# Kernel tuning notes

Measured on AMD Instinct MI355X. Metric: run time of the kernel, lower is better.

## Reference

```python
import jax, jax.numpy as jnp
import numpy as np

B, N, D, K, H, L = 4, 20000, 64, 256, 4, 2
F = 4 * D
DH = D // H
SCALE = DH ** -0.5
EPS = 1e-5


def _layernorm(x, g, b):
    m = jnp.mean(x, axis=-1, keepdims=True)
    v = jnp.mean(jnp.square(x - m), axis=-1, keepdims=True)
    return (x - m) / jnp.sqrt(v + EPS) * g + b


def setup_inputs() -> dict:
    key = jax.random.key(0)
    ks = jax.random.split(key, 12)
    s = 0.02
    return {
        'expr': jax.random.normal(ks[0], (B, N), jnp.float32),
        'emb': jax.random.normal(ks[1], (N, D), jnp.float32),
        'Wq': jax.random.normal(ks[2], (L, D, D), jnp.float32) * s,
        'Wk': jax.random.normal(ks[3], (L, D, D), jnp.float32) * s,
        'Wv': jax.random.normal(ks[4], (L, D, D), jnp.float32) * s,
        'projK': jax.random.normal(ks[5], (L, N, K), jnp.float32) * s,
        'projV': jax.random.normal(ks[6], (L, N, K), jnp.float32) * s,
        'Wo': jax.random.normal(ks[7], (L, D, D), jnp.float32) * s,
        'bo': jnp.zeros((L, D), jnp.float32),
        'g1': jnp.ones((L, D), jnp.float32),
        'be1': jnp.zeros((L, D), jnp.float32),
        'W1': jax.random.normal(ks[8], (L, D, F), jnp.float32) * s,
        'bf1': jnp.zeros((L, F), jnp.float32),
        'W2': jax.random.normal(ks[9], (L, F, D), jnp.float32) * s,
        'bf2': jnp.zeros((L, D), jnp.float32),
        'g2': jnp.ones((L, D), jnp.float32),
        'be2': jnp.zeros((L, D), jnp.float32),
    }


def _forward(expr, emb, Wq, Wk, Wv, projK, projV, Wo, bo, g1, be1, W1, bf1, W2, bf2, g2, be2):
    # gene_ids = arange(N) for every batch row -> embedding lookup is just the table
    x = emb[None, :, :] * expr[:, :, None]  # [B, N, D]
    for i in range(L):
        b = x.shape[0]
        # Linformer self-attention
        q = jnp.einsum('bnd,de->bne', x, Wq[i])                 # [B, N, D]
        k_low = jnp.einsum('bnd,nk->bkd', x, projK[i])          # [B, K, D]
        v_low = jnp.einsum('bnd,nk->bkd', x, projV[i])          # [B, K, D]
        k = jnp.einsum('bkd,de->bke', k_low, Wk[i])             # [B, K, D]
        v = jnp.einsum('bkd,de->bke', v_low, Wv[i])             # [B, K, D]
        qh = q.reshape(b, N, H, DH).transpose(0, 2, 1, 3)       # [B, H, N, DH]
        kh = k.reshape(b, K, H, DH).transpose(0, 2, 1, 3)       # [B, H, K, DH]
        vh = v.reshape(b, K, H, DH).transpose(0, 2, 1, 3)       # [B, H, K, DH]
        dots = jnp.einsum('bhnd,bhkd->bhnk', qh, kh) * SCALE    # [B, H, N, K]
        attn = jax.nn.softmax(dots, axis=-1)
        o = jnp.einsum('bhnk,bhkd->bhnd', attn, vh)             # [B, H, N, DH]
        o = o.transpose(0, 2, 1, 3).reshape(b, N, D)
        o = jnp.einsum('bnd,de->bne', o, Wo[i]) + bo[i]
        x = _layernorm(o + x, g1[i], be1[i])
        # FFN (exact GELU, matching torch nn.GELU default)
        h = jax.nn.gelu(jnp.einsum('bnd,df->bnf', x, W1[i]) + bf1[i], approximate=False)
        f = jnp.einsum('bnf,fd->bnd', h, W2[i]) + bf2[i]
        x = _layernorm(f + x, g2[i], be2[i])
    return x


def reference(expr, emb, Wq, Wk, Wv, projK, projV, Wo, bo, g1, be1, W1, bf1, W2, bf2, g2, be2):
    return _forward(expr, emb, Wq, Wk, Wv, projK, projV, Wo, bo, g1, be1, W1, bf1, W2, bf2, g2, be2)
```

## Files before the change

kernel.cpp:

```cpp
#include <hip/hip_runtime.h>

using u16 = unsigned short;
typedef __bf16 bf16x8 __attribute__((ext_vector_type(8)));
typedef u16    u16x8  __attribute__((ext_vector_type(8)));
typedef u16    u16x4  __attribute__((ext_vector_type(4)));
typedef float  f32x4  __attribute__((ext_vector_type(4)));
typedef float  f32x16 __attribute__((ext_vector_type(16)));

#define DEV static __device__ __forceinline__

constexpr int NB = 4;
constexpr int NN = 20000;
constexpr int DD = 64;
constexpr int KK = 256;
constexpr int ROWS = NB * NN;

DEV float b2f(u16 u) { union { unsigned i; float f; } c; c.i = ((unsigned)u) << 16; return c.f; }
DEV u16 f2b(float f) {
  union { float f; unsigned i; } c; c.f = f;
  unsigned i = c.i + 0x7FFFu + ((c.i >> 16) & 1u);
  return (u16)(i >> 16);
}
DEV bf16x8 ldb8(const u16* p) { return *reinterpret_cast<const bf16x8*>(p); }
DEV f32x16 mfma32(bf16x8 a, bf16x8 b, f32x16 c) { return __builtin_amdgcn_mfma_f32_32x32x16_bf16(a, b, c, 0, 0, 0); }

__global__ __launch_bounds__(256) void k_wconv(
    const float* __restrict__ Wq, const float* __restrict__ Wo,
    const float* __restrict__ W1, const float* __restrict__ W2, u16* __restrict__ wb) {
  int m = blockIdx.y, l = blockIdx.z;
  const float* src; u16* dst; int Dout, S, CT;
  if (m == 0)      { src = Wq + l * 4096;  dst = wb + l * 4096;          Dout = 64;  S = 4;  CT = 2; }
  else if (m == 1) { src = Wo + l * 4096;  dst = wb + 8192 + l * 4096;   Dout = 64;  S = 4;  CT = 2; }
  else if (m == 2) { src = W1 + l * 16384; dst = wb + 16384 + l * 16384; Dout = 256; S = 4;  CT = 8; }
  else             { src = W2 + l * 16384; dst = wb + 49152 + l * 16384; Dout = 64;  S = 16; CT = 2; }
  int slot = blockIdx.x * 256 + threadIdx.x;
  if (slot >= S * CT * 64) return;
  int s = slot / (CT * 64), rem = slot % (CT * 64);
  int ct = rem >> 6, lane = rem & 63;
  int hi = lane >> 5, lo = lane & 31;
  u16x8 o;
#pragma unroll
  for (int j = 0; j < 8; ++j) o[j] = f2b(src[(s * 16 + hi * 8 + j) * Dout + ct * 32 + lo]);
  *reinterpret_cast<u16x8*>(&dst[slot * 8]) = o;
}

__global__ __launch_bounds__(256) void k_transpose(
    const float* __restrict__ projK, const float* __restrict__ projV,
    u16* __restrict__ pKT, u16* __restrict__ pVT) {
  int nt = blockIdx.x, kt = blockIdx.y, z = blockIdx.z;
  int layer = z & 1, pv = z >> 1;
  const float* src = (pv ? projV : projK) + (size_t)layer * NN * KK;
  u16* dst = (pv ? pVT : pKT) + (size_t)layer * KK * NN;
  int n0 = nt * 64, k0 = kt * 64;
  __shared__ float lds[64][65];
  int t = threadIdx.x;
  int r = t >> 4, c4 = (t & 15) * 4;
#pragma unroll
  for (int i = 0; i < 4; ++i) {
    int rr = r + i * 16;
    float4 v = make_float4(0.f, 0.f, 0.f, 0.f);
    if (n0 + rr < NN) v = *reinterpret_cast<const float4*>(&src[(size_t)(n0 + rr) * KK + k0 + c4]);
    lds[c4 + 0][rr] = v.x; lds[c4 + 1][rr] = v.y; lds[c4 + 2][rr] = v.z; lds[c4 + 3][rr] = v.w;
  }
  __syncthreads();
  int kr = t >> 3, nb = (t & 7) * 8;
#pragma unroll
  for (int p = 0; p < 2; ++p) {
    int k = kr + p * 32;
    if (n0 + nb < NN) {
      u16x8 o;
#pragma unroll
      for (int j = 0; j < 8; ++j) o[j] = f2b(lds[k][nb + j]);
      *reinterpret_cast<u16x8*>(&dst[(size_t)(k0 + k) * NN + n0 + nb]) = o;
    }
  }
}

__global__ __launch_bounds__(256) void k_xt(const u16* __restrict__ x, u16* __restrict__ xT) {
  int nt = blockIdx.x, b = blockIdx.y;
  int n0 = nt * 64;
  __shared__ u16 lds[64][70];
  int t = threadIdx.x;
  int r = t >> 4, c4 = (t & 15) * 4;
  const u16* xb = x + (size_t)b * NN * 64;
#pragma unroll
  for (int i = 0; i < 4; ++i) {
    int rr = r + i * 16;
    u16x4 v = {};
    if (n0 + rr < NN) v = *reinterpret_cast<const u16x4*>(&xb[(size_t)(n0 + rr) * 64 + c4]);
    lds[c4 + 0][rr] = v[0]; lds[c4 + 1][rr] = v[1];
    lds[c4 + 2][rr] = v[2]; lds[c4 + 3][rr] = v[3];
  }
  __syncthreads();
  int dr = t >> 3, nb = (t & 7) * 8;
  u16* xo = xT + (size_t)b * 64 * NN;
#pragma unroll
  for (int p = 0; p < 2; ++p) {
    int d = dr + p * 32;
    if (n0 + nb < NN) {
      u16x8 o;
#pragma unroll
      for (int j = 0; j < 8; ++j) o[j] = lds[d][nb + j];
      *reinterpret_cast<u16x8*>(&xo[(size_t)d * NN + n0 + nb]) = o;
    }
  }
}

__global__ __launch_bounds__(256) void k_embed(
    const float* __restrict__ expr, const float* __restrict__ emb, u16* __restrict__ xb) {
  int idx8 = (blockIdx.x * 256 + threadIdx.x) * 8;
  int b = idx8 / (NN * DD);
  int rem = idx8 - b * (NN * DD);
  int n = rem >> 6, d = rem & 63;
  float4 e0 = *reinterpret_cast<const float4*>(&emb[(n << 6) + d]);
  float4 e1 = *reinterpret_cast<const float4*>(&emb[(n << 6) + d + 4]);
  float s = expr[b * NN + n];
  u16x8 o;
  o[0] = f2b(e0.x * s); o[1] = f2b(e0.y * s); o[2] = f2b(e0.z * s); o[3] = f2b(e0.w * s);
  o[4] = f2b(e1.x * s); o[5] = f2b(e1.y * s); o[6] = f2b(e1.z * s); o[7] = f2b(e1.w * s);
  *reinterpret_cast<u16x8*>(&xb[idx8]) = o;
}

template <int EPI>
__global__ __launch_bounds__(256) void k_gemm_64_64(
    const u16* __restrict__ A, const u16* __restrict__ WB,
    const float* __restrict__ bias, const u16* __restrict__ res,
    const float* __restrict__ g, const float* __restrict__ be, u16* __restrict__ out) {
  int t = threadIdx.x, w = t >> 6, lane = t & 63;
  int lo = lane & 31, hi = lane >> 5;
  int unit = blockIdx.x * 4 + w;
  if (unit >= ROWS / 64) return;
  bf16x8 wf[4][2];
#pragma unroll
  for (int s = 0; s < 4; ++s)
#pragma unroll
    for (int ct = 0; ct < 2; ++ct) wf[s][ct] = ldb8(&WB[((s * 2 + ct) * 64 + lane) * 8]);
  float bia[2], gg[2], bb[2];
  if (EPI) {
#pragma unroll
    for (int ct = 0; ct < 2; ++ct) {
      bia[ct] = bias[ct * 32 + lo];
      gg[ct] = g[ct * 32 + lo];
      bb[ct] = be[ct * 32 + lo];
    }
  }
  f32x16 acc[2][2] = {};
  int r0 = unit * 64;
#pragma unroll
  for (int s = 0; s < 4; ++s) {
#pragma unroll
    for (int rt = 0; rt < 2; ++rt) {
      bf16x8 a = ldb8(&A[(size_t)(r0 + rt * 32 + lo) * 64 + s * 16 + hi * 8]);
      acc[rt][0] = mfma32(a, wf[s][0], acc[rt][0]);
      acc[rt][1] = mfma32(a, wf[s][1], acc[rt][1]);
    }
  }
#pragma unroll
  for (int rt = 0; rt < 2; ++rt) {
#pragma unroll
    for (int reg = 0; reg < 16; ++reg) {
      int row = r0 + rt * 32 + (reg & 3) + 8 * (reg >> 2) + 4 * hi;
      if (EPI == 0) {
        out[(size_t)row * 64 + lo] = f2b(acc[rt][0][reg]);
        out[(size_t)row * 64 + 32 + lo] = f2b(acc[rt][1][reg]);
      } else {
        float a0 = acc[rt][0][reg] + bia[0] + b2f(res[(size_t)row * 64 + lo]);
        float a1 = acc[rt][1][reg] + bia[1] + b2f(res[(size_t)row * 64 + 32 + lo]);
        float su = a0 + a1, sq = a0 * a0 + a1 * a1;
#pragma unroll
        for (int m = 1; m <= 16; m <<= 1) { su += __shfl_xor(su, m); sq += __shfl_xor(sq, m); }
        float mean = su * (1.f / 64.f);
        float var = sq * (1.f / 64.f) - mean * mean;
        float rstd = rsqrtf(var + 1e-5f);
        out[(size_t)row * 64 + lo] = f2b((a0 - mean) * rstd * gg[0] + bb[0]);
        out[(size_t)row * 64 + 32 + lo] = f2b((a1 - mean) * rstd * gg[1] + bb[1]);
      }
    }
  }
}

__global__ __launch_bounds__(256, 2) void k_gemm_64_256(
    const u16* __restrict__ A, const u16* __restrict__ WB,
    const float* __restrict__ bias, u16* __restrict__ out) {
  int t = threadIdx.x, w = t >> 6, lane = t & 63;
  int lo = lane & 31, hi = lane >> 5;
  int colg = w & 1;
  int unit = blockIdx.x * 2 + (w >> 1);
  if (unit >= ROWS / 32) return;
  bf16x8 wf[4][4];
  float bia[4];
#pragma unroll
  for (int s = 0; s < 4; ++s)
#pragma unroll
    for (int ct = 0; ct < 4; ++ct) wf[s][ct] = ldb8(&WB[((s * 8 + colg * 4 + ct) * 64 + lane) * 8]);
#pragma unroll
  for (int ct = 0; ct < 4; ++ct) bia[ct] = bias[colg * 128 + ct * 32 + lo];
  f32x16 acc[4] = {};
  int r0 = unit * 32;
#pragma unroll
  for (int s = 0; s < 4; ++s) {
    bf16x8 a = ldb8(&A[(size_t)(r0 + lo) * 64 + s * 16 + hi * 8]);
#pragma unroll
    for (int ct = 0; ct < 4; ++ct) acc[ct] = mfma32(a, wf[s][ct], acc[ct]);
  }
#pragma unroll
  for (int ct = 0; ct < 4; ++ct) {
#pragma unroll
    for (int reg = 0; reg < 16; ++reg) {
      int row = r0 + (reg & 3) + 8 * (reg >> 2) + 4 * hi;
      float x = acc[ct][reg] + bia[ct];
      float gel = 0.5f * x * (1.f + erff(x * 0.7071067811865475f));
      out[(size_t)row * 256 + colg * 128 + ct * 32 + lo] = f2b(gel);
    }
  }
}

__global__ __launch_bounds__(256) void k_gemm_256_64(
    const u16* __restrict__ A, const u16* __restrict__ WB,
    const float* __restrict__ bias, const u16* __restrict__ res,
    const float* __restrict__ g, const float* __restrict__ be,
    u16* __restrict__ outb, float* __restrict__ outf) {
  int t = threadIdx.x, w = t >> 6, lane = t & 63;
  int lo = lane & 31, hi = lane >> 5;
  int unit = blockIdx.x * 4 + w;
  if (unit >= ROWS / 64) return;
  float bia[2], gg[2], bb[2];
#pragma unroll
  for (int ct = 0; ct < 2; ++ct) {
    bia[ct] = bias[ct * 32 + lo];
    gg[ct] = g[ct * 32 + lo];
    bb[ct] = be[ct * 32 + lo];
  }
  f32x16 acc[2][2] = {};
  int r0 = unit * 64;
#pragma unroll
  for (int s = 0; s < 16; ++s) {
    bf16x8 w0 = ldb8(&WB[((s * 2 + 0) * 64 + lane) * 8]);
    bf16x8 w1 = ldb8(&WB[((s * 2 + 1) * 64 + lane) * 8]);
#pragma unroll
    for (int rt = 0; rt < 2; ++rt) {
      bf16x8 a = ldb8(&A[(size_t)(r0 + rt * 32 + lo) * 256 + s * 16 + hi * 8]);
      acc[rt][0] = mfma32(a, w0, acc[rt][0]);
      acc[rt][1] = mfma32(a, w1, acc[rt][1]);
    }
  }
#pragma unroll
  for (int rt = 0; rt < 2; ++rt) {
#pragma unroll
    for (int reg = 0; reg < 16; ++reg) {
      int row = r0 + rt * 32 + (reg & 3) + 8 * (reg >> 2) + 4 * hi;
      float a0 = acc[rt][0][reg] + bia[0] + b2f(res[(size_t)row * 64 + lo]);
      float a1 = acc[rt][1][reg] + bia[1] + b2f(res[(size_t)row * 64 + 32 + lo]);
      float su = a0 + a1, sq = a0 * a0 + a1 * a1;
#pragma unroll
      for (int m = 1; m <= 16; m <<= 1) { su += __shfl_xor(su, m); sq += __shfl_xor(sq, m); }
      float mean = su * (1.f / 64.f);
      float var = sq * (1.f / 64.f) - mean * mean;
      float rstd = rsqrtf(var + 1e-5f);
      float o0 = (a0 - mean) * rstd * gg[0] + bb[0];
      float o1 = (a1 - mean) * rstd * gg[1] + bb[1];
      if (outb) {
        outb[(size_t)row * 64 + lo] = f2b(o0);
        outb[(size_t)row * 64 + 32 + lo] = f2b(o1);
      }
      if (outf) {
        outf[(size_t)row * 64 + lo] = o0;
        outf[(size_t)row * 64 + 32 + lo] = o1;
      }
    }
  }
}

__global__ __launch_bounds__(256) void k_proj(
    const u16* __restrict__ xT, const u16* __restrict__ pKT_l, const u16* __restrict__ pVT_l,
    float* __restrict__ part) {
  int c = blockIdx.x, b = blockIdx.y, proj = blockIdx.z;
  const u16* P = proj ? pVT_l : pKT_l;
  int t = threadIdx.x, w = t >> 6, lane = t & 63;
  int lo = lane & 31, hi = lane >> 5;
  int d0 = (w & 1) * 32;
  int kbase = (w >> 1) * 128;
  int n0 = c * 512;
  int rem = NN - n0;
  int steps = (rem < 512 ? rem : 512) >> 4;
  const u16* xr = xT + ((size_t)b * 64 + d0 + lo) * NN;
  f32x16 acc[4] = {};
  for (int s = 0; s < steps; ++s) {
    int nb = n0 + s * 16 + hi * 8;
    bf16x8 a = ldb8(&xr[nb]);
#pragma unroll
    for (int gI = 0; gI < 4; ++gI) {
      bf16x8 bfr = ldb8(&P[(size_t)(kbase + gI * 32 + lo) * NN + nb]);
      acc[gI] = mfma32(a, bfr, acc[gI]);
    }
  }
  float* dst = part + ((size_t)(proj * NB + b) * 40 + c) * (64 * 256);
#pragma unroll
  for (int gI = 0; gI < 4; ++gI)
#pragma unroll
    for (int r = 0; r < 16; ++r) {
      int d = d0 + (r & 3) + 8 * (r >> 2) + 4 * hi;
      dst[d * 256 + kbase + gI * 32 + lo] = acc[gI][r];
    }
}

__global__ __launch_bounds__(256) void k_p2(
    const float* __restrict__ part, const float* __restrict__ Wk_l, const float* __restrict__ Wv_l,
    u16* __restrict__ kbuf, u16* __restrict__ vT) {
  int ks = blockIdx.x, b = blockIdx.y, proj = blockIdx.z;
  int k0 = ks * 8;
  const float* W = proj ? Wv_l : Wk_l;
  __shared__ float low[64][8];
  int t = threadIdx.x;
  const float* src = part + (size_t)(proj * NB + b) * 40 * (64 * 256);
#pragma unroll
  for (int i = 0; i < 2; ++i) {
    int idx = i * 256 + t;
    int e = idx >> 3, k = idx & 7;
    float s = 0.f;
    for (int cc = 0; cc < 40; ++cc) s += src[(size_t)cc * (64 * 256) + e * 256 + k0 + k];
    low[e][k] = s;
  }
  __syncthreads();
#pragma unroll
  for (int i = 0; i < 2; ++i) {
    int idx = i * 256 + t;
    int d = idx & 63, kk = idx >> 6;
    float a = 0.f;
#pragma unroll
    for (int e = 0; e < 64; ++e) a += low[e][kk] * W[e * 64 + d];
    u16 o = f2b(a);
    if (proj == 0)
      kbuf[((size_t)b * KK + k0 + kk) * 64 + d] = o;
    else
      vT[((size_t)b * 64 + d) * KK + k0 + kk] = o;
  }
}

__global__ __launch_bounds__(256) void k_attn(
    const u16* __restrict__ q, const u16* __restrict__ kbuf, const u16* __restrict__ vT,
    u16* __restrict__ ao) {
  int t = threadIdx.x, w = t >> 6, lane = t & 63;
  int lo = lane & 31, hi = lane >> 5;
  int h = blockIdx.y, b = blockIdx.z;
  int n0w = blockIdx.x * 128 + w * 32;
  if (n0w >= NN) return;
  const u16* qb = q + (size_t)b * NN * 64;
  const u16* kb = kbuf + (size_t)b * KK * 64 + h * 16;
  const u16* vtb = vT + (size_t)b * 64 * KK + (size_t)(h * 16 + (lane & 15)) * KK;
  u16* aob = ao + (size_t)b * NN * 64;
  const float C = 0.25f * 1.4426950408889634f;
  bf16x8 qf = ldb8(&qb[(size_t)(n0w + lo) * 64 + h * 16 + hi * 8]);
  f32x16 acc = {};
  float ssum = 0.f;
#pragma unroll
  for (int kt = 0; kt < 8; ++kt) {
    bf16x8 kf = ldb8(&kb[(size_t)(kt * 32 + lo) * 64 + hi * 8]);
    f32x16 z = {};
    f32x16 s = mfma32(kf, qf, z);
#pragma unroll
    for (int r = 0; r < 16; ++r) { s[r] = exp2f(s[r] * C); ssum += s[r]; }
#pragma unroll
    for (int c = 0; c < 2; ++c) {
      float px[8];
#pragma unroll
      for (int j = 0; j < 8; ++j) px[j] = __shfl_xor(s[c * 8 + j], 32);
      u16x8 bu;
#pragma unroll
      for (int j = 0; j < 4; ++j) {
        bu[j] = f2b(hi ? px[4 + j] : s[c * 8 + j]);
        bu[4 + j] = f2b(hi ? s[c * 8 + 4 + j] : px[j]);
      }
      bf16x8 af = ldb8(&vtb[kt * 32 + c * 16 + hi * 8]);
      acc = mfma32(af, __builtin_bit_cast(bf16x8, bu), acc);
    }
  }
  ssum += __shfl_xor(ssum, 32);
  float inv = 1.f / ssum;
  float o[8], ox[8];
#pragma unroll
  for (int r = 0; r < 8; ++r) o[r] = acc[r] * inv;
#pragma unroll
  for (int r = 0; r < 8; ++r) ox[r] = __shfl_xor(o[r], 32);
  u16x8 st;
#pragma unroll
  for (int j = 0; j < 4; ++j) {
    st[j] = f2b(hi ? ox[4 + j] : o[j]);
    st[4 + j] = f2b(hi ? o[4 + j] : ox[j]);
  }
  *reinterpret_cast<u16x8*>(&aob[(size_t)(n0w + lo) * 64 + h * 16 + hi * 8]) = st;
}

extern "C" void kernel_launch(void* const* d_in, const int* in_sizes, int n_in,
                              void* d_out, int out_size, void* d_ws, size_t ws_size,
                              hipStream_t stream) {
  const float* expr = (const float*)d_in[0];
  const float* emb  = (const float*)d_in[1];
  const float* Wq   = (const float*)d_in[2];
  const float* Wk   = (const float*)d_in[3];
  const float* Wv   = (const float*)d_in[4];
  const float* projK = (const float*)d_in[5];
  const float* projV = (const float*)d_in[6];
  const float* Wo   = (const float*)d_in[7];
  const float* bo   = (const float*)d_in[8];
  const float* g1   = (const float*)d_in[9];
  const float* be1  = (const float*)d_in[10];
  const float* W1   = (const float*)d_in[11];
  const float* bf1  = (const float*)d_in[12];
  const float* W2   = (const float*)d_in[13];
  const float* bf2  = (const float*)d_in[14];
  const float* g2   = (const float*)d_in[15];
  const float* be2  = (const float*)d_in[16];
  float* out = (float*)d_out;
  char* ws = (char*)d_ws;

  u16* xb0 = (u16*)(ws + 0);
  u16* xb1 = (u16*)(ws + 10240000);
  u16* xb2 = (u16*)(ws + 20480000);
  u16* qb  = (u16*)(ws + 30720000);
  u16* aob = (u16*)(ws + 40960000);
  u16* hb  = (u16*)(ws + 51200000);
  float* part = (float*)(ws + 51200000);
  u16* pKT = (u16*)(ws + 92160000);
  u16* pVT = (u16*)(ws + 112640000);
  u16* xTb = (u16*)(ws + 133120000);
  u16* kB  = (u16*)(ws + 143360000);
  u16* vTB = (u16*)(ws + 143491072);
  u16* wb  = (u16*)(ws + 143622144);

  k_wconv<<<dim3(8, 4, 2), 256, 0, stream>>>(Wq, Wo, W1, W2, wb);
  k_transpose<<<dim3(313, 4, 4), 256, 0, stream>>>(projK, projV, pKT, pVT);
  k_embed<<<2500, 256, 0, stream>>>(expr, emb, xb0);

  const u16* xin = xb0;
  for (int l = 0; l < 2; ++l) {
    const u16* wbq = wb + l * 4096;
    const u16* wbo = wb + 8192 + l * 4096;
    const u16* wb1 = wb + 16384 + l * 16384;
    const u16* wb2 = wb + 49152 + l * 16384;
    k_gemm_64_64<0><<<313, 256, 0, stream>>>(xin, wbq, nullptr, nullptr, nullptr, nullptr, qb);
    k_xt<<<dim3(313, NB), 256, 0, stream>>>(xin, xTb);
    k_proj<<<dim3(40, NB, 2), 256, 0, stream>>>(xTb, pKT + (size_t)l * KK * NN, pVT + (size_t)l * KK * NN, part);
    k_p2<<<dim3(32, NB, 2), 256, 0, stream>>>(part, Wk + l * 4096, Wv + l * 4096, kB, vTB);
    k_attn<<<dim3(157, 4, NB), 256, 0, stream>>>(qb, kB, vTB, aob);
    k_gemm_64_64<1><<<313, 256, 0, stream>>>(aob, wbo, bo + l * 64, xin, g1 + l * 64, be1 + l * 64, xb1);
    k_gemm_64_256<<<1250, 256, 0, stream>>>(xb1, wb1, bf1 + l * 256, hb);
    k_gemm_256_64<<<313, 256, 0, stream>>>(hb, wb2, bf2 + l * 64, xb1,
                                           g2 + l * 64, be2 + l * 64,
                                           l == 0 ? xb2 : nullptr, l == 1 ? out : nullptr);
    xin = xb2;
  }
}
```

Baseline: 490.3 us.

## Merge preprocessing and Q/transpose kernels, streamline attention softmax, halve GEMM row tiles

Folds the weight conversion, projection transposes and embedding into one k_pre launch, and the Q projection plus x transpose into one k_qxt launch, to cut launch overhead. The attention softmax now uses exp2 with log2e·scale folded into K, packed bf16 conversion and permlane32 swaps. The row sum comes from an extra ones column in the PV MFMA. The k_proj loop is unrolled by 4 to issue more loads up front, and the 64-wide GEMMs move to 32-row units per wave with double the grid. The changes carry some risk: the ones-buffer trick depends on the V layout, and exp2 is used without max subtraction.

```diff
diff --git a/kernel.cpp b/kernel.cpp
--- a/kernel.cpp
+++ b/kernel.cpp
@@ -6,6 +6,7 @@
 typedef u16    u16x4  __attribute__((ext_vector_type(4)));
 typedef float  f32x4  __attribute__((ext_vector_type(4)));
 typedef float  f32x16 __attribute__((ext_vector_type(16)));
+typedef unsigned uint4v __attribute__((ext_vector_type(4)));
 
 #define DEV static __device__ __forceinline__
 
@@ -24,248 +25,140 @@
 DEV bf16x8 ldb8(const u16* p) { return *reinterpret_cast<const bf16x8*>(p); }
 DEV f32x16 mfma32(bf16x8 a, bf16x8 b, f32x16 c) { return __builtin_amdgcn_mfma_f32_32x32x16_bf16(a, b, c, 0, 0, 0); }
 
-__global__ __launch_bounds__(256) void k_wconv(
+DEV unsigned cvtpk(float lo, float hi) {
+  unsigned r;
+  asm("v_cvt_pk_bf16_f32 %0, %1, %2" : "=v"(r) : "v"(lo), "v"(hi));
+  return r;
+}
+DEV void swap32(unsigned& a, unsigned& b) {
+  auto r = __builtin_amdgcn_permlane32_swap((int)a, (int)b, false, false);
+  a = (unsigned)r[0]; b = (unsigned)r[1];
+}
+
+__global__ __launch_bounds__(256) void k_pre(
+    const float* __restrict__ expr, const float* __restrict__ emb,
     const float* __restrict__ Wq, const float* __restrict__ Wo,
-    const float* __restrict__ W1, const float* __restrict__ W2, u16* __restrict__ wb) {
-  int m = blockIdx.y, l = blockIdx.z;
-  const float* src; u16* dst; int Dout, S, CT;
-  if (m == 0)      { src = Wq + l * 4096;  dst = wb + l * 4096;          Dout = 64;  S = 4;  CT = 2; }
-  else if (m == 1) { src = Wo + l * 4096;  dst = wb + 8192 + l * 4096;   Dout = 64;  S = 4;  CT = 2; }
-  else if (m == 2) { src = W1 + l * 16384; dst = wb + 16384 + l * 16384; Dout = 256; S = 4;  CT = 8; }
-  else             { src = W2 + l * 16384; dst = wb + 49152 + l * 16384; Dout = 64;  S = 16; CT = 2; }
-  int slot = blockIdx.x * 256 + threadIdx.x;
-  if (slot >= S * CT * 64) return;
-  int s = slot / (CT * 64), rem = slot % (CT * 64);
-  int ct = rem >> 6, lane = rem & 63;
-  int hi = lane >> 5, lo = lane & 31;
-  u16x8 o;
-#pragma unroll
-  for (int j = 0; j < 8; ++j) o[j] = f2b(src[(s * 16 + hi * 8 + j) * Dout + ct * 32 + lo]);
-  *reinterpret_cast<u16x8*>(&dst[slot * 8]) = o;
-}
-
-__global__ __launch_bounds__(256) void k_transpose(
+    const float* __restrict__ W1, const float* __restrict__ W2,
     const float* __restrict__ projK, const float* __restrict__ projV,
-    u16* __restrict__ pKT, u16* __restrict__ pVT) {
-  int nt = blockIdx.x, kt = blockIdx.y, z = blockIdx.z;
-  int layer = z & 1, pv = z >> 1;
-  const float* src = (pv ? projV : projK) + (size_t)layer * NN * KK;
-  u16* dst = (pv ? pVT : pKT) + (size_t)layer * KK * NN;
-  int n0 = nt * 64, k0 = kt * 64;
+    u16* __restrict__ wb, u16* __restrict__ pKT, u16* __restrict__ pVT,
+    u16* __restrict__ xb, u16* __restrict__ ones) {
   __shared__ float lds[64][65];
+  int bid = blockIdx.x;
   int t = threadIdx.x;
-  int r = t >> 4, c4 = (t & 15) * 4;
-#pragma unroll
-  for (int i = 0; i < 4; ++i) {
-    int rr = r + i * 16;
-    float4 v = make_float4(0.f, 0.f, 0.f, 0.f);
-    if (n0 + rr < NN) v = *reinterpret_cast<const float4*>(&src[(size_t)(n0 + rr) * KK + k0 + c4]);
-    lds[c4 + 0][rr] = v.x; lds[c4 + 1][rr] = v.y; lds[c4 + 2][rr] = v.z; lds[c4 + 3][rr] = v.w;
-  }
-  __syncthreads();
-  int kr = t >> 3, nb = (t & 7) * 8;
-#pragma unroll
-  for (int p = 0; p < 2; ++p) {
-    int k = kr + p * 32;
-    if (n0 + nb < NN) {
-      u16x8 o;
-#pragma unroll
-      for (int j = 0; j < 8; ++j) o[j] = f2b(lds[k][nb + j]);
-      *reinterpret_cast<u16x8*>(&dst[(size_t)(k0 + k) * NN + n0 + nb]) = o;
-    }
-  }
-}
-
-__global__ __launch_bounds__(256) void k_xt(const u16* __restrict__ x, u16* __restrict__ xT) {
-  int nt = blockIdx.x, b = blockIdx.y;
-  int n0 = nt * 64;
-  __shared__ u16 lds[64][70];
+  if (bid < 5008) {
+    int nt = bid % 313, q = bid / 313, kt = q & 3, z = q >> 2;
+    int layer = z & 1, pv = z >> 1;
+    const float* src = (pv ? projV : projK) + (size_t)layer * NN * KK;
+    u16* dst = (pv ? pVT : pKT) + (size_t)layer * KK * NN;
+    int n0 = nt * 64, k0 = kt * 64;
+    int r = t >> 4, c4 = (t & 15) * 4;
+#pragma unroll
+    for (int i = 0; i < 4; ++i) {
+      int rr = r + i * 16;
+      float4 v = make_float4(0.f, 0.f, 0.f, 0.f);
+      if (n0 + rr < NN) v = *reinterpret_cast<const float4*>(&src[(size_t)(n0 + rr) * KK + k0 + c4]);
+      lds[c4 + 0][rr] = v.x; lds[c4 + 1][rr] = v.y; lds[c4 + 2][rr] = v.z; lds[c4 + 3][rr] = v.w;
+    }
+    __syncthreads();
+    int kr = t >> 3, nb = (t & 7) * 8;
+#pragma unroll
+    for (int p = 0; p < 2; ++p) {
+      int k = kr + p * 32;
+      if (n0 + nb < NN) {
+        u16x8 o;
+#pragma unroll
+        for (int j = 0; j < 8; ++j) o[j] = f2b(lds[k][nb + j]);
+        *reinterpret_cast<u16x8*>(&dst[(size_t)(k0 + k) * NN + n0 + nb]) = o;
+      }
+    }
+  } else if (bid < 7508) {
+    int idx8 = ((bid - 5008) * 256 + t) * 8;
+    int b = idx8 / (NN * DD);
+    int rem = idx8 - b * (NN * DD);
+    int n = rem >> 6, d = rem & 63;
+    float4 e0 = *reinterpret_cast<const float4*>(&emb[(n << 6) + d]);
+    float4 e1 = *reinterpret_cast<const float4*>(&emb[(n << 6) + d + 4]);
+    float s = expr[b * NN + n];
+    u16x8 o;
+    o[0] = f2b(e0.x * s); o[1] = f2b(e0.y * s); o[2] = f2b(e0.z * s); o[3] = f2b(e0.w * s);
+    o[4] = f2b(e1.x * s); o[5] = f2b(e1.y * s); o[6] = f2b(e1.z * s); o[7] = f2b(e1.w * s);
+    *reinterpret_cast<u16x8*>(&xb[idx8]) = o;
+  } else if (bid < 7572) {
+    int b2 = bid - 7508;
+    int bx = b2 & 7, m = (b2 >> 3) & 3, l = b2 >> 5;
+    const float* src; u16* dst; int Dout, S, CT;
+    if (m == 0)      { src = Wq + l * 4096;  dst = wb + l * 4096;          Dout = 64;  S = 4;  CT = 2; }
+    else if (m == 1) { src = Wo + l * 4096;  dst = wb + 8192 + l * 4096;   Dout = 64;  S = 4;  CT = 2; }
+    else if (m == 2) { src = W1 + l * 16384; dst = wb + 16384 + l * 16384; Dout = 256; S = 4;  CT = 8; }
+    else             { src = W2 + l * 16384; dst = wb + 49152 + l * 16384; Dout = 64;  S = 16; CT = 2; }
+    int slot = bx * 256 + t;
+    if (slot >= S * CT * 64) return;
+    int s = slot / (CT * 64), rem = slot % (CT * 64);
+    int ct = rem >> 6, lane = rem & 63;
+    int hi = lane >> 5, lo = lane & 31;
+    u16x8 o;
+#pragma unroll
+    for (int j = 0; j < 8; ++j) o[j] = f2b(src[(s * 16 + hi * 8 + j) * Dout + ct * 32 + lo]);
+    *reinterpret_cast<u16x8*>(&dst[slot * 8]) = o;
+  } else {
+    ones[t] = 0x3F80;
+  }
+}
+
+__global__ __launch_bounds__(256) void k_qxt(
+    const u16* __restrict__ x, const u16* __restrict__ WB,
+    u16* __restrict__ qb, u16* __restrict__ xT) {
+  __shared__ u16 ldsx[64][70];
+  int bid = blockIdx.x;
   int t = threadIdx.x;
-  int r = t >> 4, c4 = (t & 15) * 4;
-  const u16* xb = x + (size_t)b * NN * 64;
-#pragma unroll
-  for (int i = 0; i < 4; ++i) {
-    int rr = r + i * 16;
-    u16x4 v = {};
-    if (n0 + rr < NN) v = *reinterpret_cast<const u16x4*>(&xb[(size_t)(n0 + rr) * 64 + c4]);
-    lds[c4 + 0][rr] = v[0]; lds[c4 + 1][rr] = v[1];
-    lds[c4 + 2][rr] = v[2]; lds[c4 + 3][rr] = v[3];
-  }
-  __syncthreads();
-  int dr = t >> 3, nb = (t & 7) * 8;
-  u16* xo = xT + (size_t)b * 64 * NN;
-#pragma unroll
-  for (int p = 0; p < 2; ++p) {
-    int d = dr + p * 32;
-    if (n0 + nb < NN) {
-      u16x8 o;
-#pragma unroll
-      for (int j = 0; j < 8; ++j) o[j] = lds[d][nb + j];
-      *reinterpret_cast<u16x8*>(&xo[(size_t)d * NN + n0 + nb]) = o;
-    }
-  }
-}
-
-__global__ __launch_bounds__(256) void k_embed(
-    const float* __restrict__ expr, const float* __restrict__ emb, u16* __restrict__ xb) {
-  int idx8 = (blockIdx.x * 256 + threadIdx.x) * 8;
-  int b = idx8 / (NN * DD);
-  int rem = idx8 - b * (NN * DD);
-  int n = rem >> 6, d = rem & 63;
-  float4 e0 = *reinterpret_cast<const float4*>(&emb[(n << 6) + d]);
-  float4 e1 = *reinterpret_cast<const float4*>(&emb[(n << 6) + d + 4]);
-  float s = expr[b * NN + n];
-  u16x8 o;
-  o[0] = f2b(e0.x * s); o[1] = f2b(e0.y * s); o[2] = f2b(e0.z * s); o[3] = f2b(e0.w * s);
-  o[4] = f2b(e1.x * s); o[5] = f2b(e1.y * s); o[6] = f2b(e1.z * s); o[7] = f2b(e1.w * s);
-  *reinterpret_cast<u16x8*>(&xb[idx8]) = o;
-}
-
-template <int EPI>
-__global__ __launch_bounds__(256) void k_gemm_64_64(
-    const u16* __restrict__ A, const u16* __restrict__ WB,
-    const float* __restrict__ bias, const u16* __restrict__ res,
-    const float* __restrict__ g, const float* __restrict__ be, u16* __restrict__ out) {
-  int t = threadIdx.x, w = t >> 6, lane = t & 63;
-  int lo = lane & 31, hi = lane >> 5;
-  int unit = blockIdx.x * 4 + w;
-  if (unit >= ROWS / 64) return;
-  bf16x8 wf[4][2];
-#pragma unroll
-  for (int s = 0; s < 4; ++s)
-#pragma unroll
-    for (int ct = 0; ct < 2; ++ct) wf[s][ct] = ldb8(&WB[((s * 2 + ct) * 64 + lane) * 8]);
-  float bia[2], gg[2], bb[2];
-  if (EPI) {
-#pragma unroll
-    for (int ct = 0; ct < 2; ++ct) {
-      bia[ct] = bias[ct * 32 + lo];
-      gg[ct] = g[ct * 32 + lo];
-      bb[ct] = be[ct * 32 + lo];
-    }
-  }
-  f32x16 acc[2][2] = {};
-  int r0 = unit * 64;
-#pragma unroll
-  for (int s = 0; s < 4; ++s) {
-#pragma unroll
-    for (int rt = 0; rt < 2; ++rt) {
-      bf16x8 a = ldb8(&A[(size_t)(r0 + rt * 32 + lo) * 64 + s * 16 + hi * 8]);
-      acc[rt][0] = mfma32(a, wf[s][0], acc[rt][0]);
-      acc[rt][1] = mfma32(a, wf[s][1], acc[rt][1]);
-    }
-  }
-#pragma unroll
-  for (int rt = 0; rt < 2; ++rt) {
-#pragma unroll
-    for (int reg = 0; reg < 16; ++reg) {
-      int row = r0 + rt * 32 + (reg & 3) + 8 * (reg >> 2) + 4 * hi;
-      if (EPI == 0) {
-        out[(size_t)row * 64 + lo] = f2b(acc[rt][0][reg]);
-        out[(size_t)row * 64 + 32 + lo] = f2b(acc[rt][1][reg]);
-      } else {
-        float a0 = acc[rt][0][reg] + bia[0] + b2f(res[(size_t)row * 64 + lo]);
-        float a1 = acc[rt][1][reg] + bia[1] + b2f(res[(size_t)row * 64 + 32 + lo]);
-        float su = a0 + a1, sq = a0 * a0 + a1 * a1;
-#pragma unroll
-        for (int m = 1; m <= 16; m <<= 1) { su += __shfl_xor(su, m); sq += __shfl_xor(sq, m); }
-        float mean = su * (1.f / 64.f);
-        float var = sq * (1.f / 64.f) - mean * mean;
-        float rstd = rsqrtf(var + 1e-5f);
-        out[(size_t)row * 64 + lo] = f2b((a0 - mean) * rstd * gg[0] + bb[0]);
-        out[(size_t)row * 64 + 32 + lo] = f2b((a1 - mean) * rstd * gg[1] + bb[1]);
-      }
-    }
-  }
-}
-
-__global__ __launch_bounds__(256, 2) void k_gemm_64_256(
-    const u16* __restrict__ A, const u16* __restrict__ WB,
-    const float* __restrict__ bias, u16* __restrict__ out) {
-  int t = threadIdx.x, w = t >> 6, lane = t & 63;
-  int lo = lane & 31, hi = lane >> 5;
-  int colg = w & 1;
-  int unit = blockIdx.x * 2 + (w >> 1);
-  if (unit >= ROWS / 32) return;
-  bf16x8 wf[4][4];
-  float bia[4];
-#pragma unroll
-  for (int s = 0; s < 4; ++s)
-#pragma unroll
-    for (int ct = 0; ct < 4; ++ct) wf[s][ct] = ldb8(&WB[((s * 8 + colg * 4 + ct) * 64 + lane) * 8]);
-#pragma unroll
-  for (int ct = 0; ct < 4; ++ct) bia[ct] = bias[colg * 128 + ct * 32 + lo];
-  f32x16 acc[4] = {};
-  int r0 = unit * 32;
-#pragma unroll
-  for (int s = 0; s < 4; ++s) {
-    bf16x8 a = ldb8(&A[(size_t)(r0 + lo) * 64 + s * 16 + hi * 8]);
-#pragma unroll
-    for (int ct = 0; ct < 4; ++ct) acc[ct] = mfma32(a, wf[s][ct], acc[ct]);
-  }
-#pragma unroll
-  for (int ct = 0; ct < 4; ++ct) {
+  if (bid < 625) {
+    int w = t >> 6, lane = t & 63;
+    int lo = lane & 31, hi = lane >> 5;
+    int unit = bid * 4 + w;
+    bf16x8 wf[4][2];
+#pragma unroll
+    for (int s = 0; s < 4; ++s)
+#pragma unroll
+      for (int ct = 0; ct < 2; ++ct) wf[s][ct] = ldb8(&WB[((s * 2 + ct) * 64 + lane) * 8]);
+    f32x16 acc[2] = {};
+    int r0 = unit * 32;
+#pragma unroll
+    for (int s = 0; s < 4; ++s) {
+      bf16x8 a = ldb8(&x[(size_t)(r0 + lo) * 64 + s * 16 + hi * 8]);
+      acc[0] = mfma32(a, wf[s][0], acc[0]);
+      acc[1] = mfma32(a, wf[s][1], acc[1]);
+    }
 #pragma unroll
     for (int reg = 0; reg < 16; ++reg) {
       int row = r0 + (reg & 3) + 8 * (reg >> 2) + 4 * hi;
-      float x = acc[ct][reg] + bia[ct];
-      float gel = 0.5f * x * (1.f + erff(x * 0.7071067811865475f));
-      out[(size_t)row * 256 + colg * 128 + ct * 32 + lo] = f2b(gel);
-    }
-  }
-}
-
-__global__ __launch_bounds__(256) void k_gemm_256_64(
-    const u16* __restrict__ A, const u16* __restrict__ WB,
-    const float* __restrict__ bias, const u16* __restrict__ res,
-    const float* __restrict__ g, const float* __restrict__ be,
-    u16* __restrict__ outb, float* __restrict__ outf) {
-  int t = threadIdx.x, w = t >> 6, lane = t & 63;
-  int lo = lane & 31, hi = lane >> 5;
-  int unit = blockIdx.x * 4 + w;
-  if (unit >= ROWS / 64) return;
-  float bia[2], gg[2], bb[2];
-#pragma unroll
-  for (int ct = 0; ct < 2; ++ct) {
-    bia[ct] = bias[ct * 32 + lo];
-    gg[ct] = g[ct * 32 + lo];
-    bb[ct] = be[ct * 32 + lo];
-  }
-  f32x16 acc[2][2] = {};
-  int r0 = unit * 64;
-#pragma unroll
-  for (int s = 0; s < 16; ++s) {
-    bf16x8 w0 = ldb8(&WB[((s * 2 + 0) * 64 + lane) * 8]);
-    bf16x8 w1 = ldb8(&WB[((s * 2 + 1) * 64 + lane) * 8]);
-#pragma unroll
-    for (int rt = 0; rt < 2; ++rt) {
-      bf16x8 a = ldb8(&A[(size_t)(r0 + rt * 32 + lo) * 256 + s * 16 + hi * 8]);
-      acc[rt][0] = mfma32(a, w0, acc[rt][0]);
-      acc[rt][1] = mfma32(a, w1, acc[rt][1]);
-    }
-  }
-#pragma unroll
-  for (int rt = 0; rt < 2; ++rt) {
-#pragma unroll
-    for (int reg = 0; reg < 16; ++reg) {
-      int row = r0 + rt * 32 + (reg & 3) + 8 * (reg >> 2) + 4 * hi;
-      float a0 = acc[rt][0][reg] + bia[0] + b2f(res[(size_t)row * 64 + lo]);
-      float a1 = acc[rt][1][reg] + bia[1] + b2f(res[(size_t)row * 64 + 32 + lo]);
-      float su = a0 + a1, sq = a0 * a0 + a1 * a1;
-#pragma unroll
-      for (int m = 1; m <= 16; m <<= 1) { su += __shfl_xor(su, m); sq += __shfl_xor(sq, m); }
-      float mean = su * (1.f / 64.f);
-      float var = sq * (1.f / 64.f) - mean * mean;
-      float rstd = rsqrtf(var + 1e-5f);
-      float o0 = (a0 - mean) * rstd * gg[0] + bb[0];
-      float o1 = (a1 - mean) * rstd * gg[1] + bb[1];
-      if (outb) {
-        outb[(size_t)row * 64 + lo] = f2b(o0);
-        outb[(size_t)row * 64 + 32 + lo] = f2b(o1);
-      }
-      if (outf) {
-        outf[(size_t)row * 64 + lo] = o0;
-        outf[(size_t)row * 64 + 32 + lo] = o1;
+      qb[(size_t)row * 64 + lo] = f2b(acc[0][reg]);
+      qb[(size_t)row * 64 + 32 + lo] = f2b(acc[1][reg]);
+    }
+  } else {
+    int v = bid - 625;
+    int nt = v % 313, b = v / 313;
+    int n0 = nt * 64;
+    int r = t >> 4, c4 = (t & 15) * 4;
+    const u16* xbp = x + (size_t)b * NN * 64;
+#pragma unroll
+    for (int i = 0; i < 4; ++i) {
+      int rr = r + i * 16;
+      u16x4 vv = {};
+      if (n0 + rr < NN) vv = *reinterpret_cast<const u16x4*>(&xbp[(size_t)(n0 + rr) * 64 + c4]);
+      ldsx[c4 + 0][rr] = vv[0]; ldsx[c4 + 1][rr] = vv[1];
+      ldsx[c4 + 2][rr] = vv[2]; ldsx[c4 + 3][rr] = vv[3];
+    }
+    __syncthreads();
+    int dr = t >> 3, nb = (t & 7) * 8;
+    u16* xo = xT + (size_t)b * 64 * NN;
+#pragma unroll
+    for (int p = 0; p < 2; ++p) {
+      int d = dr + p * 32;
+      if (n0 + nb < NN) {
+        u16x8 o;
+#pragma unroll
+        for (int j = 0; j < 8; ++j) o[j] = ldsx[d][nb + j];
+        *reinterpret_cast<u16x8*>(&xo[(size_t)d * NN + n0 + nb]) = o;
       }
     }
   }
@@ -285,22 +178,34 @@
   int steps = (rem < 512 ? rem : 512) >> 4;
   const u16* xr = xT + ((size_t)b * 64 + d0 + lo) * NN;
   f32x16 acc[4] = {};
-  for (int s = 0; s < steps; ++s) {
+  int s = 0;
+  for (; s + 4 <= steps; s += 4) {
+    bf16x8 a[4]; bf16x8 bv[4][4];
+#pragma unroll
+    for (int u = 0; u < 4; ++u) {
+      int nb = n0 + (s + u) * 16 + hi * 8;
+      a[u] = ldb8(&xr[nb]);
+#pragma unroll
+      for (int g = 0; g < 4; ++g) bv[u][g] = ldb8(&P[(size_t)(kbase + g * 32 + lo) * NN + nb]);
+    }
+#pragma unroll
+    for (int u = 0; u < 4; ++u)
+#pragma unroll
+      for (int g = 0; g < 4; ++g) acc[g] = mfma32(a[u], bv[u][g], acc[g]);
+  }
+  for (; s < steps; ++s) {
     int nb = n0 + s * 16 + hi * 8;
     bf16x8 a = ldb8(&xr[nb]);
 #pragma unroll
-    for (int gI = 0; gI < 4; ++gI) {
-      bf16x8 bfr = ldb8(&P[(size_t)(kbase + gI * 32 + lo) * NN + nb]);
-      acc[gI] = mfma32(a, bfr, acc[gI]);
-    }
+    for (int g = 0; g < 4; ++g) acc[g] = mfma32(a, ldb8(&P[(size_t)(kbase + g * 32 + lo) * NN + nb]), acc[g]);
   }
   float* dst = part + ((size_t)(proj * NB + b) * 40 + c) * (64 * 256);
 #pragma unroll
-  for (int gI = 0; gI < 4; ++gI)
+  for (int g = 0; g < 4; ++g)
 #pragma unroll
     for (int r = 0; r < 16; ++r) {
       int d = d0 + (r & 3) + 8 * (r >> 2) + 4 * hi;
-      dst[d * 256 + kbase + gI * 32 + lo] = acc[gI][r];
+      dst[d * 256 + kbase + g * 32 + lo] = acc[g][r];
     }
 }
 
@@ -329,66 +234,188 @@
     float a = 0.f;
 #pragma unroll
     for (int e = 0; e < 64; ++e) a += low[e][kk] * W[e * 64 + d];
-    u16 o = f2b(a);
-    if (proj == 0)
-      kbuf[((size_t)b * KK + k0 + kk) * 64 + d] = o;
-    else
-      vT[((size_t)b * 64 + d) * KK + k0 + kk] = o;
+    if (proj == 0) {
+      kbuf[((size_t)b * KK + k0 + kk) * 64 + d] = f2b(a * 0.3606737602222409f);
+    } else {
+      vT[((size_t)b * 64 + d) * KK + k0 + kk] = f2b(a);
+    }
   }
 }
 
 __global__ __launch_bounds__(256) void k_attn(
     const u16* __restrict__ q, const u16* __restrict__ kbuf, const u16* __restrict__ vT,
-    u16* __restrict__ ao) {
-  int t = threadIdx.x, w = t >> 6, lane = t & 63;
+    const u16* __restrict__ ones, u16* __restrict__ ao) {
+  int t = threadIdx.x, h = t >> 6, lane = t & 63;
   int lo = lane & 31, hi = lane >> 5;
-  int h = blockIdx.y, b = blockIdx.z;
-  int n0w = blockIdx.x * 128 + w * 32;
-  if (n0w >= NN) return;
+  int b = blockIdx.y;
+  int n0 = blockIdx.x * 32;
   const u16* qb = q + (size_t)b * NN * 64;
   const u16* kb = kbuf + (size_t)b * KK * 64 + h * 16;
-  const u16* vtb = vT + (size_t)b * 64 * KK + (size_t)(h * 16 + (lane & 15)) * KK;
-  u16* aob = ao + (size_t)b * NN * 64;
-  const float C = 0.25f * 1.4426950408889634f;
-  bf16x8 qf = ldb8(&qb[(size_t)(n0w + lo) * 64 + h * 16 + hi * 8]);
+  const u16* vsrc = (lo < 16)
+      ? vT + (size_t)b * 64 * KK + (size_t)(h * 16 + lo) * KK
+      : ones;
+  bf16x8 qf = ldb8(&qb[(size_t)(n0 + lo) * 64 + h * 16 + hi * 8]);
   f32x16 acc = {};
-  float ssum = 0.f;
 #pragma unroll
   for (int kt = 0; kt < 8; ++kt) {
     bf16x8 kf = ldb8(&kb[(size_t)(kt * 32 + lo) * 64 + hi * 8]);
     f32x16 z = {};
     f32x16 s = mfma32(kf, qf, z);
-#pragma unroll
-    for (int r = 0; r < 16; ++r) { s[r] = exp2f(s[r] * C); ssum += s[r]; }
+    float e[16];
+#pragma unroll
+    for (int r = 0; r < 16; ++r) e[r] = __builtin_amdgcn_exp2f(s[r]);
 #pragma unroll
     for (int c = 0; c < 2; ++c) {
-      float px[8];
-#pragma unroll
-      for (int j = 0; j < 8; ++j) px[j] = __shfl_xor(s[c * 8 + j], 32);
-      u16x8 bu;
-#pragma unroll
-      for (int j = 0; j < 4; ++j) {
-        bu[j] = f2b(hi ? px[4 + j] : s[c * 8 + j]);
-        bu[4 + j] = f2b(hi ? s[c * 8 + 4 + j] : px[j]);
-      }
-      bf16x8 af = ldb8(&vtb[kt * 32 + c * 16 + hi * 8]);
-      acc = mfma32(af, __builtin_bit_cast(bf16x8, bu), acc);
-    }
-  }
-  ssum += __shfl_xor(ssum, 32);
-  float inv = 1.f / ssum;
-  float o[8], ox[8];
+      unsigned Aw = cvtpk(e[c * 8 + 0], e[c * 8 + 1]);
+      unsigned Bw = cvtpk(e[c * 8 + 2], e[c * 8 + 3]);
+      unsigned Cw = cvtpk(e[c * 8 + 4], e[c * 8 + 5]);
+      unsigned Dw = cvtpk(e[c * 8 + 6], e[c * 8 + 7]);
+      swap32(Aw, Cw);
+      swap32(Bw, Dw);
+      uint4v pk; pk.x = Aw; pk.y = Bw; pk.z = Cw; pk.w = Dw;
+      bf16x8 af = ldb8(&vsrc[kt * 32 + c * 16 + hi * 8]);
+      acc = mfma32(af, __builtin_bit_cast(bf16x8, pk), acc);
+    }
+  }
+  float inv = __builtin_amdgcn_rcpf(acc[8]);
+  float o[8];
 #pragma unroll
   for (int r = 0; r < 8; ++r) o[r] = acc[r] * inv;
-#pragma unroll
-  for (int r = 0; r < 8; ++r) ox[r] = __shfl_xor(o[r], 32);
-  u16x8 st;
-#pragma unroll
-  for (int j = 0; j < 4; ++j) {
-    st[j] = f2b(hi ? ox[4 + j] : o[j]);
-    st[4 + j] = f2b(hi ? o[4 + j] : ox[j]);
-  }
-  *reinterpret_cast<u16x8*>(&aob[(size_t)(n0w + lo) * 64 + h * 16 + hi * 8]) = st;
+  unsigned Aw = cvtpk(o[0], o[1]);
+  unsigned Bw = cvtpk(o[2], o[3]);
+  unsigned Cw = cvtpk(o[4], o[5]);
+  unsigned Dw = cvtpk(o[6], o[7]);
+  swap32(Aw, Cw);
+  swap32(Bw, Dw);
+  uint4v st; st.x = Aw; st.y = Bw; st.z = Cw; st.w = Dw;
+  *reinterpret_cast<uint4v*>(&ao[(size_t)b * NN * 64 + (size_t)(n0 + lo) * 64 + h * 16 + hi * 8]) = st;
+}
+
+__global__ __launch_bounds__(256) void k_oln(
+    const u16* __restrict__ A, const u16* __restrict__ WB,
+    const float* __restrict__ bias, const u16* __restrict__ res,
+    const float* __restrict__ g, const float* __restrict__ be, u16* __restrict__ out) {
+  int t = threadIdx.x, w = t >> 6, lane = t & 63;
+  int lo = lane & 31, hi = lane >> 5;
+  int unit = blockIdx.x * 4 + w;
+  bf16x8 wf[4][2];
+#pragma unroll
+  for (int s = 0; s < 4; ++s)
+#pragma unroll
+    for (int ct = 0; ct < 2; ++ct) wf[s][ct] = ldb8(&WB[((s * 2 + ct) * 64 + lane) * 8]);
+  float bia[2], gg[2], bb[2];
+#pragma unroll
+  for (int ct = 0; ct < 2; ++ct) {
+    bia[ct] = bias[ct * 32 + lo];
+    gg[ct] = g[ct * 32 + lo];
+    bb[ct] = be[ct * 32 + lo];
+  }
+  f32x16 acc[2] = {};
+  int r0 = unit * 32;
+#pragma unroll
+  for (int s = 0; s < 4; ++s) {
+    bf16x8 a = ldb8(&A[(size_t)(r0 + lo) * 64 + s * 16 + hi * 8]);
+    acc[0] = mfma32(a, wf[s][0], acc[0]);
+    acc[1] = mfma32(a, wf[s][1], acc[1]);
+  }
+#pragma unroll
+  for (int reg = 0; reg < 16; ++reg) {
+    int row = r0 + (reg & 3) + 8 * (reg >> 2) + 4 * hi;
+    float a0 = acc[0][reg] + bia[0] + b2f(res[(size_t)row * 64 + lo]);
+    float a1 = acc[1][reg] + bia[1] + b2f(res[(size_t)row * 64 + 32 + lo]);
+    float su = a0 + a1, sq = a0 * a0 + a1 * a1;
+#pragma unroll
+    for (int m = 1; m <= 16; m <<= 1) { su += __shfl_xor(su, m); sq += __shfl_xor(sq, m); }
+    float mean = su * (1.f / 64.f);
+    float var = sq * (1.f / 64.f) - mean * mean;
+    float rstd = rsqrtf(var + 1e-5f);
+    out[(size_t)row * 64 + lo] = f2b((a0 - mean) * rstd * gg[0] + bb[0]);
+    out[(size_t)row * 64 + 32 + lo] = f2b((a1 - mean) * rstd * gg[1] + bb[1]);
+  }
+}
+
+__global__ __launch_bounds__(256, 2) void k_gemm_64_256(
+    const u16* __restrict__ A, const u16* __restrict__ WB,
+    const float* __restrict__ bias, u16* __restrict__ out) {
+  int t = threadIdx.x, w = t >> 6, lane = t & 63;
+  int lo = lane & 31, hi = lane >> 5;
+  int colg = w & 1;
+  int unit = blockIdx.x * 2 + (w >> 1);
+  bf16x8 wf[4][4];
+  float bia[4];
+#pragma unroll
+  for (int s = 0; s < 4; ++s)
+#pragma unroll
+    for (int ct = 0; ct < 4; ++ct) wf[s][ct] = ldb8(&WB[((s * 8 + colg * 4 + ct) * 64 + lane) * 8]);
+#pragma unroll
+  for (int ct = 0; ct < 4; ++ct) bia[ct] = bias[colg * 128 + ct * 32 + lo];
+  f32x16 acc[4] = {};
+  int r0 = unit * 32;
+#pragma unroll
+  for (int s = 0; s < 4; ++s) {
+    bf16x8 a = ldb8(&A[(size_t)(r0 + lo) * 64 + s * 16 + hi * 8]);
+#pragma unroll
+    for (int ct = 0; ct < 4; ++ct) acc[ct] = mfma32(a, wf[s][ct], acc[ct]);
+  }
+#pragma unroll
+  for (int ct = 0; ct < 4; ++ct) {
+#pragma unroll
+    for (int reg = 0; reg < 16; ++reg) {
+      int row = r0 + (reg & 3) + 8 * (reg >> 2) + 4 * hi;
+      float x = acc[ct][reg] + bia[ct];
+      float gel = 0.5f * x * (1.f + erff(x * 0.7071067811865475f));
+      out[(size_t)row * 256 + colg * 128 + ct * 32 + lo] = f2b(gel);
+    }
+  }
+}
+
+__global__ __launch_bounds__(256) void k_gemm_256_64(
+    const u16* __restrict__ A, const u16* __restrict__ WB,
+    const float* __restrict__ bias, const u16* __restrict__ res,
+    const float* __restrict__ g, const float* __restrict__ be,
+    u16* __restrict__ outb, float* __restrict__ outf) {
+  int t = threadIdx.x, w = t >> 6, lane = t & 63;
+  int lo = lane & 31, hi = lane >> 5;
+  int unit = blockIdx.x * 4 + w;
+  float bia[2], gg[2], bb[2];
+#pragma unroll
+  for (int ct = 0; ct < 2; ++ct) {
+    bia[ct] = bias[ct * 32 + lo];
+    gg[ct] = g[ct * 32 + lo];
+    bb[ct] = be[ct * 32 + lo];
+  }
+  f32x16 acc[2] = {};
+  int r0 = unit * 32;
+#pragma unroll
+  for (int s = 0; s < 16; ++s) {
+    bf16x8 w0 = ldb8(&WB[((s * 2 + 0) * 64 + lane) * 8]);
+    bf16x8 w1 = ldb8(&WB[((s * 2 + 1) * 64 + lane) * 8]);
+    bf16x8 a = ldb8(&A[(size_t)(r0 + lo) * 256 + s * 16 + hi * 8]);
+    acc[0] = mfma32(a, w0, acc[0]);
+    acc[1] = mfma32(a, w1, acc[1]);
+  }
+#pragma unroll
+  for (int reg = 0; reg < 16; ++reg) {
+    int row = r0 + (reg & 3) + 8 * (reg >> 2) + 4 * hi;
+    float a0 = acc[0][reg] + bia[0] + b2f(res[(size_t)row * 64 + lo]);
+    float a1 = acc[1][reg] + bia[1] + b2f(res[(size_t)row * 64 + 32 + lo]);
+    float su = a0 + a1, sq = a0 * a0 + a1 * a1;
+#pragma unroll
+    for (int m = 1; m <= 16; m <<= 1) { su += __shfl_xor(su, m); sq += __shfl_xor(sq, m); }
+    float mean = su * (1.f / 64.f);
+    float var = sq * (1.f / 64.f) - mean * mean;
+    float rstd = rsqrtf(var + 1e-5f);
+    float o0 = (a0 - mean) * rstd * gg[0] + bb[0];
+    float o1 = (a1 - mean) * rstd * gg[1] + bb[1];
+    if (outb) {
+      outb[(size_t)row * 64 + lo] = f2b(o0);
+      outb[(size_t)row * 64 + 32 + lo] = f2b(o1);
+    }
+    if (outf) {
+      outf[(size_t)row * 64 + lo] = o0;
+      outf[(size_t)row * 64 + 32 + lo] = o1;
+    }
+  }
 }
 
 extern "C" void kernel_launch(void* const* d_in, const int* in_sizes, int n_in,
@@ -427,10 +454,10 @@
   u16* kB  = (u16*)(ws + 143360000);
   u16* vTB = (u16*)(ws + 143491072);
   u16* wb  = (u16*)(ws + 143622144);
-
-  k_wconv<<<dim3(8, 4, 2), 256, 0, stream>>>(Wq, Wo, W1, W2, wb);
-  k_transpose<<<dim3(313, 4, 4), 256, 0, stream>>>(projK, projV, pKT, pVT);
-  k_embed<<<2500, 256, 0, stream>>>(expr, emb, xb0);
+  u16* ones = (u16*)(ws + 143785984);
+
+  k_pre<<<7573, 256, 0, stream>>>(expr, emb, Wq, Wo, W1, W2, projK, projV,
+                                  wb, pKT, pVT, xb0, ones);
 
   const u16* xin = xb0;
   for (int l = 0; l < 2; ++l) {
@@ -438,14 +465,13 @@
     const u16* wbo = wb + 8192 + l * 4096;
     const u16* wb1 = wb + 16384 + l * 16384;
     const u16* wb2 = wb + 49152 + l * 16384;
-    k_gemm_64_64<0><<<313, 256, 0, stream>>>(xin, wbq, nullptr, nullptr, nullptr, nullptr, qb);
-    k_xt<<<dim3(313, NB), 256, 0, stream>>>(xin, xTb);
+    k_qxt<<<1877, 256, 0, stream>>>(xin, wbq, qb, xTb);
     k_proj<<<dim3(40, NB, 2), 256, 0, stream>>>(xTb, pKT + (size_t)l * KK * NN, pVT + (size_t)l * KK * NN, part);
     k_p2<<<dim3(32, NB, 2), 256, 0, stream>>>(part, Wk + l * 4096, Wv + l * 4096, kB, vTB);
-    k_attn<<<dim3(157, 4, NB), 256, 0, stream>>>(qb, kB, vTB, aob);
-    k_gemm_64_64<1><<<313, 256, 0, stream>>>(aob, wbo, bo + l * 64, xin, g1 + l * 64, be1 + l * 64, xb1);
+    k_attn<<<dim3(625, NB), 256, 0, stream>>>(qb, kB, vTB, ones, aob);
+    k_oln<<<625, 256, 0, stream>>>(aob, wbo, bo + l * 64, xin, g1 + l * 64, be1 + l * 64, xb1);
     k_gemm_64_256<<<1250, 256, 0, stream>>>(xb1, wb1, bf1 + l * 256, hb);
-    k_gemm_256_64<<<313, 256, 0, stream>>>(hb, wb2, bf2 + l * 64, xb1,
+    k_gemm_256_64<<<625, 256, 0, stream>>>(hb, wb2, bf2 + l * 64, xb1,
                                            g2 + l * 64, be2 + l * 64,
                                            l == 0 ? xb2 : nullptr, l == 1 ? out : nullptr);
     xin = xb2;
```

Result: faster. 421.9 us (-13.9%).
